# Kernel optimization log

Measured on AMD Instinct MI355X. Metric: run time of the kernel, lower is better.

## Reference

```python
import jax, jax.numpy as jnp
import numpy as np

D = 512
B = 16
T = 16384
LN_EPS = 1e-5


def setup_inputs() -> dict:
    key = jax.random.key(0)
    ks = jax.random.split(key, 16)
    s = 0.02
    return {
        "x": jax.random.normal(ks[0], (B, D), jnp.float32),
        "lfb_feats": jax.random.normal(ks[1], (B, T, D), jnp.float32),
        "w_theta": jax.random.normal(ks[2], (D, D), jnp.float32) * s,
        "b_theta": jnp.zeros((D,), jnp.float32),
        "w_phi": jax.random.normal(ks[3], (D, D), jnp.float32) * s,
        "b_phi": jnp.zeros((D,), jnp.float32),
        "w_gi": jax.random.normal(ks[4], (D, D), jnp.float32) * s,
        "b_gi": jnp.zeros((D,), jnp.float32),
        "ln_g": jnp.ones((D,), jnp.float32),
        "ln_b": jnp.zeros((D,), jnp.float32),
        "w_fc": jax.random.normal(ks[5], (D, D), jnp.float32) * s,
        "b_fc": jnp.zeros((D,), jnp.float32),
        "w_nlb": jax.random.normal(ks[6], (2 * D, 2 * D), jnp.float32) * s,
        "b_nlb": jnp.zeros((2 * D,), jnp.float32),
        "w1": jax.random.normal(ks[7], (1, D), jnp.float32) * s,
        "b1": jnp.zeros((1,), jnp.float32),
        "w2": jax.random.normal(ks[8], (1, D), jnp.float32) * s,
        "b2": jnp.zeros((1,), jnp.float32),
    }


def _layernorm(h, g, b):
    mu = jnp.mean(h, axis=-1, keepdims=True)
    var = jnp.var(h, axis=-1, keepdims=True)
    return (h - mu) * jax.lax.rsqrt(var + LN_EPS) * g + b


def reference(x, lfb_feats, w_theta, b_theta, w_phi, b_phi, w_gi, b_gi,
              ln_g, ln_b, w_fc, b_fc, w_nlb, b_nlb, w1, b1, w2, b2):
    d = x.shape[-1]
    scale = jnp.sqrt(jnp.asarray(d, x.dtype))  # 1/sqrt(1/D) == sqrt(D), per source
    # 1x1 conv projections == dense matmuls
    theta = x @ w_theta.T + b_theta                      # [B, D] (single query)
    phi = lfb_feats @ w_phi.T + b_phi                    # [B, T, D]
    gi = lfb_feats @ w_gi.T + b_gi                       # [B, T, D]
    scores = jnp.einsum('bd,btd->bt', theta, phi) * scale  # [B, T]
    attn = jax.nn.softmax(scores, axis=-1)
    ctx = jnp.einsum('bt,btd->bd', attn, gi)             # [B, D]
    h = jax.nn.relu(_layernorm(ctx, ln_g, ln_b))
    h = h @ w_fc.T + b_fc                                # 1x1 conv fc; dropout = identity (eval)
    longterm = h + x                                     # residual with input feats
    feats = jnp.concatenate([x, longterm], axis=-1)      # [B, 2D]
    feats = jax.nn.relu(jax.nn.relu(feats) @ w_nlb.T + b_nlb)
    pred1 = feats[:, :d] @ w1.T + b1                     # [B, 1]
    pred2 = feats[:, d:] @ w2.T + b2                     # [B, 1]
    return jnp.concatenate([pred1, pred2], axis=1)       # [B, 2]
```

## Files before the change

kernel.cpp:

```cpp
#include <hip/hip_runtime.h>
#include <math.h>

#define D     512
#define BSZ   16
#define TLEN  16384
#define ROWS  128
#define CHUNKS (TLEN / ROWS)
#define LN_EPS 1e-5f
#define SCALE 22.627416997969522f

typedef float v4 __attribute__((ext_vector_type(4)));

__device__ float g_theta[BSZ * D];
__device__ float g_u[BSZ * D];
__device__ float g_pm[BSZ * CHUNKS];
__device__ float g_pl[BSZ * CHUNKS];
__device__ float g_pv[(size_t)BSZ * CHUNKS * D];
__device__ float g_ctx[BSZ * D];
__device__ float g_feats[BSZ * 2 * D];
__device__ float g_gact[BSZ * 2 * D];

__global__ __launch_bounds__(256) void k_theta(const float* __restrict__ x,
                                               const float* __restrict__ w_theta,
                                               const float* __restrict__ b_theta) {
  __shared__ float x_sm[D];
  const int b = blockIdx.y, t = threadIdx.x;
  x_sm[t] = x[b * D + t];
  x_sm[t + 256] = x[b * D + t + 256];
  __syncthreads();
  const int d = blockIdx.x * 256 + t;
  const float4* wrow = (const float4*)(w_theta + (size_t)d * D);
  float acc = b_theta[d];
#pragma unroll 8
  for (int e4 = 0; e4 < D / 4; ++e4) {
    float4 w4 = wrow[e4];
    acc += w4.x * x_sm[4 * e4] + w4.y * x_sm[4 * e4 + 1] +
           w4.z * x_sm[4 * e4 + 2] + w4.w * x_sm[4 * e4 + 3];
  }
  g_theta[b * D + d] = acc;
}

__global__ __launch_bounds__(256) void k_u(const float* __restrict__ w_phi) {
  __shared__ float th_sm[D];
  const int b = blockIdx.y, t = threadIdx.x;
  th_sm[t] = g_theta[b * D + t];
  th_sm[t + 256] = g_theta[b * D + t + 256];
  __syncthreads();
  const int e = blockIdx.x * 256 + t;
  float acc = 0.f;
#pragma unroll 8
  for (int d = 0; d < D; ++d) acc += th_sm[d] * w_phi[(size_t)d * D + e];
  g_u[b * D + e] = acc * SCALE;
}

__global__ __launch_bounds__(256) void k_attn(const float* __restrict__ lfb) {
  const int b = blockIdx.y, chunk = blockIdx.x;
  const int tid = threadIdx.x, lane = tid & 63, wave = tid >> 6;

  const v4* urow = (const v4*)(g_u + b * D);
  const v4 u0 = urow[lane];
  const v4 u1 = urow[64 + lane];

  float m = -INFINITY, l = 0.f;
  v4 va = {0.f, 0.f, 0.f, 0.f};
  v4 vb = {0.f, 0.f, 0.f, 0.f};

  const float* base = lfb + ((size_t)b * TLEN + (size_t)chunk * ROWS) * D;
  for (int i = 0; i < ROWS / 4; ++i) {
    const v4* row = (const v4*)(base + (size_t)(i * 4 + wave) * D);
    v4 a = __builtin_nontemporal_load(row + lane);
    v4 c = __builtin_nontemporal_load(row + 64 + lane);
    v4 p = a * u0 + c * u1;
    float s = p.x + p.y + p.z + p.w;
#pragma unroll
    for (int off = 32; off > 0; off >>= 1) s += __shfl_xor(s, off);
    if (s > m) {
      float alpha = __expf(m - s);
      l = l * alpha + 1.f;
      va = va * alpha + a;
      vb = vb * alpha + c;
      m = s;
    } else {
      float w = __expf(s - m);
      l += w;
      va += a * w;
      vb += c * w;
    }
  }

  __shared__ float wm[4], wl[4];
  __shared__ float wv[4][D];
  ((v4*)wv[wave])[lane] = va;
  ((v4*)wv[wave])[64 + lane] = vb;
  if (lane == 0) { wm[wave] = m; wl[wave] = l; }
  __syncthreads();

  const float bm = fmaxf(fmaxf(wm[0], wm[1]), fmaxf(wm[2], wm[3]));
  const float f0 = __expf(wm[0] - bm), f1 = __expf(wm[1] - bm);
  const float f2 = __expf(wm[2] - bm), f3 = __expf(wm[3] - bm);
  const size_t pidx = (size_t)b * CHUNKS + chunk;
#pragma unroll
  for (int k = 0; k < 2; ++k) {
    int p = tid + k * 256;
    g_pv[pidx * D + p] =
        f0 * wv[0][p] + f1 * wv[1][p] + f2 * wv[2][p] + f3 * wv[3][p];
  }
  if (tid == 0) {
    g_pm[pidx] = bm;
    g_pl[pidx] = f0 * wl[0] + f1 * wl[1] + f2 * wl[2] + f3 * wl[3];
  }
}

__global__ __launch_bounds__(256) void k_ctx(const float* __restrict__ w_gi,
                                             const float* __restrict__ b_gi) {
  __shared__ float v_sm[D];
  const int b = blockIdx.y, t = threadIdx.x;
  const float* pm = g_pm + b * CHUNKS;
  const float* pl = g_pl + b * CHUNKS;
  const float* pv = g_pv + (size_t)b * CHUNKS * D;
  float bm = -INFINITY;
  for (int c = 0; c < CHUNKS; ++c) bm = fmaxf(bm, pm[c]);
  float lg = 0.f, a0 = 0.f, a1 = 0.f;
  for (int c = 0; c < CHUNKS; ++c) {
    float f = __expf(pm[c] - bm);
    lg += f * pl[c];
    a0 += f * pv[(size_t)c * D + t];
    a1 += f * pv[(size_t)c * D + t + 256];
  }
  const float invl = 1.f / lg;
  v_sm[t] = a0 * invl;
  v_sm[t + 256] = a1 * invl;
  __syncthreads();
  const int d = blockIdx.x * 256 + t;
  const float4* wrow = (const float4*)(w_gi + (size_t)d * D);
  float acc = b_gi[d];
#pragma unroll 8
  for (int e4 = 0; e4 < D / 4; ++e4) {
    float4 w4 = wrow[e4];
    acc += w4.x * v_sm[4 * e4] + w4.y * v_sm[4 * e4 + 1] +
           w4.z * v_sm[4 * e4 + 2] + w4.w * v_sm[4 * e4 + 3];
  }
  g_ctx[b * D + d] = acc;
}

__global__ __launch_bounds__(256) void k_lnfc(const float* __restrict__ ln_g,
                                              const float* __restrict__ ln_b,
                                              const float* __restrict__ w_fc,
                                              const float* __restrict__ b_fc,
                                              const float* __restrict__ x) {
  __shared__ float h_sm[D];
  __shared__ float rs[4], rq[4];
  const int b = blockIdx.y, t = threadIdx.x;
  const float c0 = g_ctx[b * D + t], c1 = g_ctx[b * D + t + 256];
  float s = c0 + c1, sq = c0 * c0 + c1 * c1;
#pragma unroll
  for (int off = 32; off > 0; off >>= 1) {
    s += __shfl_xor(s, off);
    sq += __shfl_xor(sq, off);
  }
  if ((t & 63) == 0) { rs[t >> 6] = s; rq[t >> 6] = sq; }
  __syncthreads();
  const float mu = (rs[0] + rs[1] + rs[2] + rs[3]) * (1.f / D);
  const float var = (rq[0] + rq[1] + rq[2] + rq[3]) * (1.f / D) - mu * mu;
  const float rstd = rsqrtf(var + LN_EPS);
  h_sm[t] = fmaxf((c0 - mu) * rstd * ln_g[t] + ln_b[t], 0.f);
  h_sm[t + 256] = fmaxf((c1 - mu) * rstd * ln_g[t + 256] + ln_b[t + 256], 0.f);
  __syncthreads();
  const int d = blockIdx.x * 256 + t;
  const float4* wrow = (const float4*)(w_fc + (size_t)d * D);
  float acc = b_fc[d];
#pragma unroll 8
  for (int e4 = 0; e4 < D / 4; ++e4) {
    float4 w4 = wrow[e4];
    acc += w4.x * h_sm[4 * e4] + w4.y * h_sm[4 * e4 + 1] +
           w4.z * h_sm[4 * e4 + 2] + w4.w * h_sm[4 * e4 + 3];
  }
  const float xv = x[b * D + d];
  g_feats[(size_t)b * 2 * D + d] = xv;
  g_feats[(size_t)b * 2 * D + D + d] = acc + xv;
}

__global__ __launch_bounds__(256) void k_nlb(const float* __restrict__ w_nlb,
                                             const float* __restrict__ b_nlb) {
  __shared__ float f_sm[2 * D];
  const int b = blockIdx.y, t = threadIdx.x;
#pragma unroll
  for (int k = 0; k < 4; ++k)
    f_sm[t + k * 256] = fmaxf(g_feats[(size_t)b * 2 * D + t + k * 256], 0.f);
  __syncthreads();
  const int j = blockIdx.x * 256 + t;
  const float4* wrow = (const float4*)(w_nlb + (size_t)j * 2 * D);
  float acc = b_nlb[j];
#pragma unroll 8
  for (int e4 = 0; e4 < 2 * D / 4; ++e4) {
    float4 w4 = wrow[e4];
    acc += w4.x * f_sm[4 * e4] + w4.y * f_sm[4 * e4 + 1] +
           w4.z * f_sm[4 * e4 + 2] + w4.w * f_sm[4 * e4 + 3];
  }
  g_gact[(size_t)b * 2 * D + j] = fmaxf(acc, 0.f);
}

__global__ __launch_bounds__(256) void k_pred(const float* __restrict__ w1,
                                              const float* __restrict__ b1,
                                              const float* __restrict__ w2,
                                              const float* __restrict__ b2,
                                              float* __restrict__ out) {
  __shared__ float rs[4], rq[4];
  const int b = blockIdx.x, t = threadIdx.x;
  const float* gb = g_gact + (size_t)b * 2 * D;
  float p1 = gb[t] * w1[t] + gb[t + 256] * w1[t + 256];
  float p2 = gb[D + t] * w2[t] + gb[D + t + 256] * w2[t + 256];
#pragma unroll
  for (int off = 32; off > 0; off >>= 1) {
    p1 += __shfl_xor(p1, off);
    p2 += __shfl_xor(p2, off);
  }
  if ((t & 63) == 0) { rs[t >> 6] = p1; rq[t >> 6] = p2; }
  __syncthreads();
  if (t == 0) {
    out[b * 2 + 0] = rs[0] + rs[1] + rs[2] + rs[3] + b1[0];
    out[b * 2 + 1] = rq[0] + rq[1] + rq[2] + rq[3] + b2[0];
  }
}

extern "C" void kernel_launch(void* const* d_in, const int* in_sizes, int n_in,
                              void* d_out, int out_size, void* d_ws,
                              size_t ws_size, hipStream_t stream) {
  const float* x       = (const float*)d_in[0];
  const float* lfb     = (const float*)d_in[1];
  const float* w_theta = (const float*)d_in[2];
  const float* b_theta = (const float*)d_in[3];
  const float* w_phi   = (const float*)d_in[4];
  const float* w_gi    = (const float*)d_in[6];
  const float* b_gi    = (const float*)d_in[7];
  const float* ln_g    = (const float*)d_in[8];
  const float* ln_b    = (const float*)d_in[9];
  const float* w_fc    = (const float*)d_in[10];
  const float* b_fc    = (const float*)d_in[11];
  const float* w_nlb   = (const float*)d_in[12];
  const float* b_nlb   = (const float*)d_in[13];
  const float* w1      = (const float*)d_in[14];
  const float* b1      = (const float*)d_in[15];
  const float* w2      = (const float*)d_in[16];
  const float* b2      = (const float*)d_in[17];
  float* out = (float*)d_out;

  k_theta<<<dim3(2, BSZ), 256, 0, stream>>>(x, w_theta, b_theta);
  k_u<<<dim3(2, BSZ), 256, 0, stream>>>(w_phi);
  k_attn<<<dim3(CHUNKS, BSZ), 256, 0, stream>>>(lfb);
  k_ctx<<<dim3(2, BSZ), 256, 0, stream>>>(w_gi, b_gi);
  k_lnfc<<<dim3(2, BSZ), 256, 0, stream>>>(ln_g, ln_b, w_fc, b_fc, x);
  k_nlb<<<dim3(4, BSZ), 256, 0, stream>>>(w_nlb, b_nlb);
  k_pred<<<BSZ, 256, 0, stream>>>(w1, b1, w2, b2, out);
}
```

Measured before the change: 806.2 us.

## Batch small GEMVs across all rows per block and unroll attention row loop

The small dense projections (theta, u, gi, fc, nlb) now stage all 16 batch rows in shared memory, and each weight row is reused across batch rows. Before, weights were re-read once per batch. The combine step and the layernorm are split into separate kernels, and the relu on the concat input is precomputed. The attention stream loop handles two rows per wave per iteration to raise memory-level parallelism. The cost is more kernel launches and fewer blocks for the small kernels, which lowers parallelism in those stages.

```diff
diff --git a/kernel.cpp b/kernel.cpp
--- a/kernel.cpp
+++ b/kernel.cpp
@@ -11,46 +11,67 @@
 
 typedef float v4 __attribute__((ext_vector_type(4)));
 
-__device__ float g_theta[BSZ * D];
-__device__ float g_u[BSZ * D];
-__device__ float g_pm[BSZ * CHUNKS];
-__device__ float g_pl[BSZ * CHUNKS];
-__device__ float g_pv[(size_t)BSZ * CHUNKS * D];
-__device__ float g_ctx[BSZ * D];
-__device__ float g_feats[BSZ * 2 * D];
-__device__ float g_gact[BSZ * 2 * D];
+__device__ __align__(16) float g_theta[BSZ * D];
+__device__ __align__(16) float g_u[BSZ * D];
+__device__ __align__(16) float g_pm[BSZ * CHUNKS];
+__device__ __align__(16) float g_pl[BSZ * CHUNKS];
+__device__ __align__(16) float g_pv[BSZ * CHUNKS * D];
+__device__ __align__(16) float g_v[BSZ * D];
+__device__ __align__(16) float g_ctx[BSZ * D];
+__device__ __align__(16) float g_h[BSZ * D];
+__device__ __align__(16) float g_rf[BSZ * 2 * D];
+__device__ __align__(16) float g_gact[BSZ * 2 * D];
 
 __global__ __launch_bounds__(256) void k_theta(const float* __restrict__ x,
                                                const float* __restrict__ w_theta,
                                                const float* __restrict__ b_theta) {
-  __shared__ float x_sm[D];
-  const int b = blockIdx.y, t = threadIdx.x;
-  x_sm[t] = x[b * D + t];
-  x_sm[t + 256] = x[b * D + t + 256];
-  __syncthreads();
-  const int d = blockIdx.x * 256 + t;
-  const float4* wrow = (const float4*)(w_theta + (size_t)d * D);
-  float acc = b_theta[d];
+  __shared__ float xs[BSZ][D];
+  const int t = threadIdx.x;
+  {
+    const float4* xg = (const float4*)x;
+    float4* xl = (float4*)&xs[0][0];
+#pragma unroll
+    for (int k = 0; k < 8; ++k) xl[k * 256 + t] = xg[k * 256 + t];
+  }
+  __syncthreads();
+  const int r = t & 31, bg = t >> 5;
+  const int row = blockIdx.x * 32 + r;
+  const float4* wrow = (const float4*)(w_theta + (size_t)row * D);
+  float acc0 = 0.f, acc1 = 0.f;
+#pragma unroll 4
+  for (int e = 0; e < D / 4; ++e) {
+    float4 w = wrow[e];
+    const float* p0 = &xs[bg][e * 4];
+    const float* p1 = &xs[bg + 8][e * 4];
+    acc0 += w.x * p0[0] + w.y * p0[1] + w.z * p0[2] + w.w * p0[3];
+    acc1 += w.x * p1[0] + w.y * p1[1] + w.z * p1[2] + w.w * p1[3];
+  }
+  const float bb = b_theta[row];
+  g_theta[bg * D + row] = acc0 + bb;
+  g_theta[(bg + 8) * D + row] = acc1 + bb;
+}
+
+__global__ __launch_bounds__(256) void k_u(const float* __restrict__ w_phi) {
+  __shared__ float th[BSZ][D];
+  const int t = threadIdx.x;
+  {
+    const float4* tg = (const float4*)g_theta;
+    float4* tl = (float4*)&th[0][0];
+#pragma unroll
+    for (int k = 0; k < 8; ++k) tl[k * 256 + t] = tg[k * 256 + t];
+  }
+  __syncthreads();
+  const int ei = t & 31, bg = t >> 5;
+  const int e = blockIdx.x * 32 + ei;
+  float acc0 = 0.f, acc1 = 0.f;
 #pragma unroll 8
-  for (int e4 = 0; e4 < D / 4; ++e4) {
-    float4 w4 = wrow[e4];
-    acc += w4.x * x_sm[4 * e4] + w4.y * x_sm[4 * e4 + 1] +
-           w4.z * x_sm[4 * e4 + 2] + w4.w * x_sm[4 * e4 + 3];
-  }
-  g_theta[b * D + d] = acc;
-}
-
-__global__ __launch_bounds__(256) void k_u(const float* __restrict__ w_phi) {
-  __shared__ float th_sm[D];
-  const int b = blockIdx.y, t = threadIdx.x;
-  th_sm[t] = g_theta[b * D + t];
-  th_sm[t + 256] = g_theta[b * D + t + 256];
-  __syncthreads();
-  const int e = blockIdx.x * 256 + t;
-  float acc = 0.f;
-#pragma unroll 8
-  for (int d = 0; d < D; ++d) acc += th_sm[d] * w_phi[(size_t)d * D + e];
-  g_u[b * D + e] = acc * SCALE;
+  for (int d = 0; d < D; ++d) {
+    float w = w_phi[(size_t)d * D + e];
+    acc0 += th[bg][d] * w;
+    acc1 += th[bg + 8][d] * w;
+  }
+  g_u[bg * D + e] = acc0 * SCALE;
+  g_u[(bg + 8) * D + e] = acc1 * SCALE;
 }
 
 __global__ __launch_bounds__(256) void k_attn(const float* __restrict__ lfb) {
@@ -66,25 +87,35 @@
   v4 vb = {0.f, 0.f, 0.f, 0.f};
 
   const float* base = lfb + ((size_t)b * TLEN + (size_t)chunk * ROWS) * D;
-  for (int i = 0; i < ROWS / 4; ++i) {
-    const v4* row = (const v4*)(base + (size_t)(i * 4 + wave) * D);
-    v4 a = __builtin_nontemporal_load(row + lane);
-    v4 c = __builtin_nontemporal_load(row + 64 + lane);
-    v4 p = a * u0 + c * u1;
-    float s = p.x + p.y + p.z + p.w;
-#pragma unroll
-    for (int off = 32; off > 0; off >>= 1) s += __shfl_xor(s, off);
-    if (s > m) {
-      float alpha = __expf(m - s);
-      l = l * alpha + 1.f;
-      va = va * alpha + a;
-      vb = vb * alpha + c;
-      m = s;
+  for (int i = 0; i < ROWS / 8; ++i) {
+    const v4* r0 = (const v4*)(base + (size_t)(i * 8 + wave * 2) * D);
+    const v4* r1 = r0 + (D / 4);
+    v4 a0 = __builtin_nontemporal_load(r0 + lane);
+    v4 c0 = __builtin_nontemporal_load(r0 + 64 + lane);
+    v4 a1 = __builtin_nontemporal_load(r1 + lane);
+    v4 c1 = __builtin_nontemporal_load(r1 + 64 + lane);
+    v4 p0 = a0 * u0 + c0 * u1;
+    v4 p1 = a1 * u0 + c1 * u1;
+    float s0 = p0.x + p0.y + p0.z + p0.w;
+    float s1 = p1.x + p1.y + p1.z + p1.w;
+#pragma unroll
+    for (int off = 32; off > 0; off >>= 1) {
+      s0 += __shfl_xor(s0, off);
+      s1 += __shfl_xor(s1, off);
+    }
+    if (s0 > m) {
+      float al = __expf(m - s0);
+      l = l * al + 1.f; va = va * al + a0; vb = vb * al + c0; m = s0;
     } else {
-      float w = __expf(s - m);
-      l += w;
-      va += a * w;
-      vb += c * w;
+      float w = __expf(s0 - m);
+      l += w; va += a0 * w; vb += c0 * w;
+    }
+    if (s1 > m) {
+      float al = __expf(m - s1);
+      l = l * al + 1.f; va = va * al + a1; vb = vb * al + c1; m = s1;
+    } else {
+      float w = __expf(s1 - m);
+      l += w; va += a1 * w; vb += c1 * w;
     }
   }
 
@@ -111,10 +142,8 @@
   }
 }
 
-__global__ __launch_bounds__(256) void k_ctx(const float* __restrict__ w_gi,
-                                             const float* __restrict__ b_gi) {
-  __shared__ float v_sm[D];
-  const int b = blockIdx.y, t = threadIdx.x;
+__global__ __launch_bounds__(256) void k_comb() {
+  const int b = blockIdx.x, t = threadIdx.x;
   const float* pm = g_pm + b * CHUNKS;
   const float* pl = g_pl + b * CHUNKS;
   const float* pv = g_pv + (size_t)b * CHUNKS * D;
@@ -127,30 +156,44 @@
     a0 += f * pv[(size_t)c * D + t];
     a1 += f * pv[(size_t)c * D + t + 256];
   }
-  const float invl = 1.f / lg;
-  v_sm[t] = a0 * invl;
-  v_sm[t + 256] = a1 * invl;
-  __syncthreads();
-  const int d = blockIdx.x * 256 + t;
-  const float4* wrow = (const float4*)(w_gi + (size_t)d * D);
-  float acc = b_gi[d];
-#pragma unroll 8
-  for (int e4 = 0; e4 < D / 4; ++e4) {
-    float4 w4 = wrow[e4];
-    acc += w4.x * v_sm[4 * e4] + w4.y * v_sm[4 * e4 + 1] +
-           w4.z * v_sm[4 * e4 + 2] + w4.w * v_sm[4 * e4 + 3];
-  }
-  g_ctx[b * D + d] = acc;
-}
-
-__global__ __launch_bounds__(256) void k_lnfc(const float* __restrict__ ln_g,
-                                              const float* __restrict__ ln_b,
-                                              const float* __restrict__ w_fc,
-                                              const float* __restrict__ b_fc,
-                                              const float* __restrict__ x) {
-  __shared__ float h_sm[D];
+  const float inv = 1.f / lg;
+  g_v[b * D + t] = a0 * inv;
+  g_v[b * D + t + 256] = a1 * inv;
+}
+
+__global__ __launch_bounds__(256) void k_gi(const float* __restrict__ w_gi,
+                                            const float* __restrict__ b_gi) {
+  __shared__ float vs[BSZ][D];
+  const int t = threadIdx.x;
+  {
+    const float4* vg = (const float4*)g_v;
+    float4* vl = (float4*)&vs[0][0];
+#pragma unroll
+    for (int k = 0; k < 8; ++k) vl[k * 256 + t] = vg[k * 256 + t];
+  }
+  __syncthreads();
+  const int r = t & 31, bg = t >> 5;
+  const int row = blockIdx.x * 32 + r;
+  const float4* wrow = (const float4*)(w_gi + (size_t)row * D);
+  float acc0 = 0.f, acc1 = 0.f;
+#pragma unroll 4
+  for (int e = 0; e < D / 4; ++e) {
+    float4 w = wrow[e];
+    const float* p0 = &vs[bg][e * 4];
+    const float* p1 = &vs[bg + 8][e * 4];
+    acc0 += w.x * p0[0] + w.y * p0[1] + w.z * p0[2] + w.w * p0[3];
+    acc1 += w.x * p1[0] + w.y * p1[1] + w.z * p1[2] + w.w * p1[3];
+  }
+  const float bb = b_gi[row];
+  g_ctx[bg * D + row] = acc0 + bb;
+  g_ctx[(bg + 8) * D + row] = acc1 + bb;
+}
+
+__global__ __launch_bounds__(256) void k_ln(const float* __restrict__ ln_g,
+                                            const float* __restrict__ ln_b,
+                                            const float* __restrict__ x) {
   __shared__ float rs[4], rq[4];
-  const int b = blockIdx.y, t = threadIdx.x;
+  const int b = blockIdx.x, t = threadIdx.x;
   const float c0 = g_ctx[b * D + t], c1 = g_ctx[b * D + t + 256];
   float s = c0 + c1, sq = c0 * c0 + c1 * c1;
 #pragma unroll
@@ -163,41 +206,69 @@
   const float mu = (rs[0] + rs[1] + rs[2] + rs[3]) * (1.f / D);
   const float var = (rq[0] + rq[1] + rq[2] + rq[3]) * (1.f / D) - mu * mu;
   const float rstd = rsqrtf(var + LN_EPS);
-  h_sm[t] = fmaxf((c0 - mu) * rstd * ln_g[t] + ln_b[t], 0.f);
-  h_sm[t + 256] = fmaxf((c1 - mu) * rstd * ln_g[t + 256] + ln_b[t + 256], 0.f);
-  __syncthreads();
-  const int d = blockIdx.x * 256 + t;
-  const float4* wrow = (const float4*)(w_fc + (size_t)d * D);
-  float acc = b_fc[d];
-#pragma unroll 8
-  for (int e4 = 0; e4 < D / 4; ++e4) {
-    float4 w4 = wrow[e4];
-    acc += w4.x * h_sm[4 * e4] + w4.y * h_sm[4 * e4 + 1] +
-           w4.z * h_sm[4 * e4 + 2] + w4.w * h_sm[4 * e4 + 3];
-  }
-  const float xv = x[b * D + d];
-  g_feats[(size_t)b * 2 * D + d] = xv;
-  g_feats[(size_t)b * 2 * D + D + d] = acc + xv;
+  g_h[b * D + t] = fmaxf((c0 - mu) * rstd * ln_g[t] + ln_b[t], 0.f);
+  g_h[b * D + t + 256] =
+      fmaxf((c1 - mu) * rstd * ln_g[t + 256] + ln_b[t + 256], 0.f);
+  g_rf[b * 2 * D + t] = fmaxf(x[b * D + t], 0.f);
+  g_rf[b * 2 * D + t + 256] = fmaxf(x[b * D + t + 256], 0.f);
+}
+
+__global__ __launch_bounds__(256) void k_fc(const float* __restrict__ w_fc,
+                                            const float* __restrict__ b_fc,
+                                            const float* __restrict__ x) {
+  __shared__ float hs[BSZ][D];
+  const int t = threadIdx.x;
+  {
+    const float4* hg = (const float4*)g_h;
+    float4* hl = (float4*)&hs[0][0];
+#pragma unroll
+    for (int k = 0; k < 8; ++k) hl[k * 256 + t] = hg[k * 256 + t];
+  }
+  __syncthreads();
+  const int r = t & 31, bg = t >> 5;
+  const int row = blockIdx.x * 32 + r;
+  const float4* wrow = (const float4*)(w_fc + (size_t)row * D);
+  float acc0 = 0.f, acc1 = 0.f;
+#pragma unroll 4
+  for (int e = 0; e < D / 4; ++e) {
+    float4 w = wrow[e];
+    const float* p0 = &hs[bg][e * 4];
+    const float* p1 = &hs[bg + 8][e * 4];
+    acc0 += w.x * p0[0] + w.y * p0[1] + w.z * p0[2] + w.w * p0[3];
+    acc1 += w.x * p1[0] + w.y * p1[1] + w.z * p1[2] + w.w * p1[3];
+  }
+  const float bb = b_fc[row];
+  g_rf[bg * 2 * D + D + row] = fmaxf(acc0 + bb + x[bg * D + row], 0.f);
+  g_rf[(bg + 8) * 2 * D + D + row] =
+      fmaxf(acc1 + bb + x[(bg + 8) * D + row], 0.f);
 }
 
 __global__ __launch_bounds__(256) void k_nlb(const float* __restrict__ w_nlb,
                                              const float* __restrict__ b_nlb) {
-  __shared__ float f_sm[2 * D];
-  const int b = blockIdx.y, t = threadIdx.x;
-#pragma unroll
-  for (int k = 0; k < 4; ++k)
-    f_sm[t + k * 256] = fmaxf(g_feats[(size_t)b * 2 * D + t + k * 256], 0.f);
-  __syncthreads();
-  const int j = blockIdx.x * 256 + t;
-  const float4* wrow = (const float4*)(w_nlb + (size_t)j * 2 * D);
-  float acc = b_nlb[j];
-#pragma unroll 8
-  for (int e4 = 0; e4 < 2 * D / 4; ++e4) {
-    float4 w4 = wrow[e4];
-    acc += w4.x * f_sm[4 * e4] + w4.y * f_sm[4 * e4 + 1] +
-           w4.z * f_sm[4 * e4 + 2] + w4.w * f_sm[4 * e4 + 3];
-  }
-  g_gact[(size_t)b * 2 * D + j] = fmaxf(acc, 0.f);
+  __shared__ float fs[BSZ][2 * D];
+  const int t = threadIdx.x;
+  {
+    const float4* fg = (const float4*)g_rf;
+    float4* fl = (float4*)&fs[0][0];
+#pragma unroll
+    for (int k = 0; k < 16; ++k) fl[k * 256 + t] = fg[k * 256 + t];
+  }
+  __syncthreads();
+  const int r = t & 31, bg = t >> 5;
+  const int row = blockIdx.x * 32 + r;
+  const float4* wrow = (const float4*)(w_nlb + (size_t)row * 2 * D);
+  float acc0 = 0.f, acc1 = 0.f;
+#pragma unroll 4
+  for (int e = 0; e < 2 * D / 4; ++e) {
+    float4 w = wrow[e];
+    const float* p0 = &fs[bg][e * 4];
+    const float* p1 = &fs[bg + 8][e * 4];
+    acc0 += w.x * p0[0] + w.y * p0[1] + w.z * p0[2] + w.w * p0[3];
+    acc1 += w.x * p1[0] + w.y * p1[1] + w.z * p1[2] + w.w * p1[3];
+  }
+  const float bb = b_nlb[row];
+  g_gact[bg * 2 * D + row] = fmaxf(acc0 + bb, 0.f);
+  g_gact[(bg + 8) * 2 * D + row] = fmaxf(acc1 + bb, 0.f);
 }
 
 __global__ __launch_bounds__(256) void k_pred(const float* __restrict__ w1,
@@ -245,11 +316,13 @@
   const float* b2      = (const float*)d_in[17];
   float* out = (float*)d_out;
 
-  k_theta<<<dim3(2, BSZ), 256, 0, stream>>>(x, w_theta, b_theta);
-  k_u<<<dim3(2, BSZ), 256, 0, stream>>>(w_phi);
+  k_theta<<<16, 256, 0, stream>>>(x, w_theta, b_theta);
+  k_u<<<16, 256, 0, stream>>>(w_phi);
   k_attn<<<dim3(CHUNKS, BSZ), 256, 0, stream>>>(lfb);
-  k_ctx<<<dim3(2, BSZ), 256, 0, stream>>>(w_gi, b_gi);
-  k_lnfc<<<dim3(2, BSZ), 256, 0, stream>>>(ln_g, ln_b, w_fc, b_fc, x);
-  k_nlb<<<dim3(4, BSZ), 256, 0, stream>>>(w_nlb, b_nlb);
+  k_comb<<<BSZ, 256, 0, stream>>>();
+  k_gi<<<16, 256, 0, stream>>>(w_gi, b_gi);
+  k_ln<<<BSZ, 256, 0, stream>>>(ln_g, ln_b, x);
+  k_fc<<<16, 256, 0, stream>>>(w_fc, b_fc, x);
+  k_nlb<<<32, 256, 0, stream>>>(w_nlb, b_nlb);
   k_pred<<<BSZ, 256, 0, stream>>>(w1, b1, w2, b2, out);
 }
```

Result: slower. 831.8 us (+3.2%).
